# Kernel tuning notes

Hardware: AMD Instinct MI355X
Metric: run time of the kernel (lower is better)

## Reference

```python
import jax, jax.numpy as jnp
import numpy as np

B, C, H, W = 8, 512, 64, 64
C8 = C // 8


def setup_inputs() -> dict:
    key = jax.random.key(0)
    ks = jax.random.split(key, 9)
    s = 1.0 / np.sqrt(C)
    return {
        "view1": jax.random.normal(ks[0], (B, C, H, W), jnp.float32),
        "view2": jax.random.normal(ks[1], (B, C, H, W), jnp.float32),
        "Wq": jax.random.normal(ks[2], (C8, C), jnp.float32) * s,
        "bq": jax.random.normal(ks[3], (C8,), jnp.float32) * 0.01,
        "Wk": jax.random.normal(ks[4], (C8, C), jnp.float32) * s,
        "bk": jax.random.normal(ks[5], (C8,), jnp.float32) * 0.01,
        "Wv": jax.random.normal(ks[6], (C, C), jnp.float32) * s,
        "bv": jax.random.normal(ks[7], (C,), jnp.float32) * 0.01,
        "gamma": jnp.array([0.5], jnp.float32),  # nn.Parameter(zeros(1)) in torch; nonzero here for nontrivial output
    }


def reference(view1, view2, Wq, bq, Wk, bk, Wv, bv, gamma):
    b, c, h, w = view1.shape
    n = h * w
    # 1x1 convs == per-pixel linear over channel dim
    q = jnp.einsum("bchw,oc->bohw", view1, Wq) + bq[None, :, None, None]
    k = jnp.einsum("bchw,oc->bohw", view2, Wk) + bk[None, :, None, None]
    v = jnp.einsum("bchw,oc->bohw", view2, Wv) + bv[None, :, None, None]
    q = q.reshape(b, -1, n).transpose(0, 2, 1)  # (B, N, C/8)
    k = k.reshape(b, -1, n)                      # (B, C/8, N)
    v = v.reshape(b, c, n)                       # (B, C, N)
    # no scaling, matching the original module
    attn = jax.nn.softmax(jnp.einsum("bnd,bdm->bnm", q, k), axis=-1)  # (B, N, N)
    out = jnp.einsum("bcn,bmn->bcm", v, attn).reshape(b, c, h, w)
    return gamma[0] * out + view1
```

## Files before the change

### kernel.cpp

```cpp
#include <hip/hip_runtime.h>

#define NB 8
#define NC 512
#define NPIX 4096
#define LOG2E 1.44269504088896340736f
#define C0TERM 28.853900817779268f

typedef __attribute__((ext_vector_type(4))) float f32x4;
typedef __attribute__((ext_vector_type(8))) short bf16x8;
typedef __attribute__((ext_vector_type(4))) unsigned short u16x4;

static __device__ __forceinline__ short f2bf(float f){
    union { float f; unsigned u; } v; v.f = f;
    unsigned r = v.u + 0x7fffu + ((v.u >> 16) & 1u);
    return (short)(r >> 16);
}

static __device__ __forceinline__ void gload16(const void* g, void* l){
    __builtin_amdgcn_global_load_lds(
        (const __attribute__((address_space(1))) char*)g,
        (__attribute__((address_space(3))) char*)l, 16, 0, 0);
}

#define VW8 asm volatile("s_waitcnt vmcnt(8)" ::: "memory")
#define VW0 asm volatile("s_waitcnt vmcnt(0)" ::: "memory")
#define BAR __builtin_amdgcn_s_barrier()
#define SB0 __builtin_amdgcn_sched_barrier(0)

__global__ void k_wconv(const float* __restrict__ wq, const float* __restrict__ wk,
                        const float* __restrict__ wv,
                        short* __restrict__ wqb, short* __restrict__ wkb,
                        short* __restrict__ wvb){
    int i = blockIdx.x * 256 + threadIdx.x;
    if (i < 64*NC){ wqb[i] = f2bf(wq[i]); wkb[i] = f2bf(wk[i]); }
    if (i < NC*NC){ wvb[i] = f2bf(wv[i]); }
}

__global__ __launch_bounds__(256) void k_projq(const float* __restrict__ X,
                                               const short* __restrict__ W,
                                               const float* __restrict__ bias,
                                               short* __restrict__ out){
    const int b = blockIdx.y;
    const int wv = threadIdx.x >> 6;
    const int lane = threadIdx.x & 63;
    const int g = lane >> 4, c16 = lane & 15;
    const int n0w = blockIdx.x * 64 + wv * 16;
    const float* Xb = X + (size_t)b * NC * NPIX;

    f32x4 acc[4];
#pragma unroll
    for (int f = 0; f < 4; ++f) acc[f] = (f32x4){0.f,0.f,0.f,0.f};

    for (int c0 = 0; c0 < NC; c0 += 32){
        bf16x8 a;
#pragma unroll
        for (int j = 0; j < 8; ++j)
            a[j] = f2bf(Xb[(size_t)(c0 + 8*g + j) * NPIX + n0w + c16]);
#pragma unroll
        for (int f = 0; f < 4; ++f){
            bf16x8 bfr = *(const bf16x8*)(W + (size_t)(f*16 + c16) * NC + c0 + 8*g);
            acc[f] = __builtin_amdgcn_mfma_f32_16x16x32_bf16(a, bfr, acc[f], 0, 0, 0);
        }
    }
#pragma unroll
    for (int f = 0; f < 4; ++f){
        int o = f*16 + c16;
        float bo = bias[o];
#pragma unroll
        for (int i = 0; i < 4; ++i)
            out[((size_t)b*NPIX + n0w + 4*g + i)*64 + o] = f2bf(acc[f][i] + bo);
    }
}

__global__ __launch_bounds__(256) void k_trans(const float* __restrict__ X,
                                               short* __restrict__ Xt){
    __shared__ __align__(16) short T[64][72];
    const int n0 = blockIdx.x * 64;
    const int c0 = blockIdx.y * 64;
    const int b  = blockIdx.z;
    const int t  = threadIdx.x;
    {
        const int cl = t >> 2;
        const int nq = (t & 3) * 16;
        const float* src = X + ((size_t)b*NC + c0 + cl)*NPIX + n0 + nq;
#pragma unroll
        for (int q = 0; q < 4; ++q){
            f32x4 v = *(const f32x4*)(src + q*4);
#pragma unroll
            for (int i = 0; i < 4; ++i)
                T[nq + q*4 + i][cl] = f2bf(v[i]);
        }
    }
    __syncthreads();
    {
        const int n  = t >> 2;
        const int cs = (t & 3) * 16;
        short* dst = Xt + ((size_t)b*NPIX + n0 + n)*NC + c0 + cs;
        *(f32x4*)dst       = *(const f32x4*)&T[n][cs];
        *(f32x4*)(dst + 8) = *(const f32x4*)&T[n][cs + 8];
    }
}

__global__ __launch_bounds__(256) void k_projv(const short* __restrict__ Xt,
                                               const short* __restrict__ W,
                                               const float* __restrict__ bias,
                                               short* __restrict__ vout){
    const int o0 = blockIdx.x * 128;
    const int n0 = blockIdx.y * 128;
    const int b  = blockIdx.z;
    const int wv = threadIdx.x >> 6;
    const int lane = threadIdx.x & 63;
    const int g = lane >> 4, c16 = lane & 15;
    const int wo = wv & 1, wn = wv >> 1;

    const short* Xb = Xt + ((size_t)b*NPIX + n0 + wn*64)*NC;
    const short* Wb = W + (size_t)(o0 + wo*64)*NC;

    f32x4 acc[4][4];
#pragma unroll
    for (int nf = 0; nf < 4; ++nf)
#pragma unroll
        for (int of = 0; of < 4; ++of) acc[nf][of] = (f32x4){0.f,0.f,0.f,0.f};

    for (int c0 = 0; c0 < NC; c0 += 32){
        bf16x8 af[4], bf_[4];
#pragma unroll
        for (int f = 0; f < 4; ++f){
            af[f]  = *(const bf16x8*)(Xb + (size_t)(f*16 + c16)*NC + c0 + 8*g);
            bf_[f] = *(const bf16x8*)(Wb + (size_t)(f*16 + c16)*NC + c0 + 8*g);
        }
#pragma unroll
        for (int nf = 0; nf < 4; ++nf)
#pragma unroll
            for (int of = 0; of < 4; ++of)
                acc[nf][of] = __builtin_amdgcn_mfma_f32_16x16x32_bf16(af[nf], bf_[of], acc[nf][of], 0,0,0);
    }

#pragma unroll
    for (int of = 0; of < 4; ++of){
        int o = o0 + wo*64 + of*16 + c16;
        float bo = bias[o];
#pragma unroll
        for (int nf = 0; nf < 4; ++nf){
            int n = n0 + wn*64 + nf*16 + 4*g;
            u16x4 pk;
#pragma unroll
            for (int i = 0; i < 4; ++i) pk[i] = (unsigned short)f2bf(acc[nf][of][i] + bo);
            *(u16x4*)(vout + ((size_t)b*NC + o)*NPIX + n) = pk;
        }
    }
}

__global__ __launch_bounds__(256) void k_projk(const short* __restrict__ Xt,
                                               const short* __restrict__ W,
                                               const float* __restrict__ bias,
                                               short* __restrict__ kout){
    const int n0 = blockIdx.x * 256;
    const int b  = blockIdx.y;
    const int wv = threadIdx.x >> 6;
    const int lane = threadIdx.x & 63;
    const int g = lane >> 4, c16 = lane & 15;

    const short* Xb = Xt + ((size_t)b*NPIX + n0 + wv*64)*NC;

    f32x4 acc[4][4];
#pragma unroll
    for (int of = 0; of < 4; ++of)
#pragma unroll
        for (int nf = 0; nf < 4; ++nf) acc[of][nf] = (f32x4){0.f,0.f,0.f,0.f};

    for (int c0 = 0; c0 < NC; c0 += 32){
        bf16x8 af[4], bf_[4];
#pragma unroll
        for (int f = 0; f < 4; ++f){
            af[f]  = *(const bf16x8*)(W + (size_t)(f*16 + c16)*NC + c0 + 8*g);
            bf_[f] = *(const bf16x8*)(Xb + (size_t)(f*16 + c16)*NC + c0 + 8*g);
        }
#pragma unroll
        for (int of = 0; of < 4; ++of)
#pragma unroll
            for (int nf = 0; nf < 4; ++nf)
                acc[of][nf] = __builtin_amdgcn_mfma_f32_16x16x32_bf16(af[of], bf_[nf], acc[of][nf], 0,0,0);
    }

#pragma unroll
    for (int nf = 0; nf < 4; ++nf){
        int n = n0 + wv*64 + nf*16 + c16;
#pragma unroll
        for (int of = 0; of < 4; ++of){
            int o = of*16 + 4*g;
            u16x4 pk;
#pragma unroll
            for (int i = 0; i < 4; ++i) pk[i] = (unsigned short)f2bf(acc[of][nf][i] + bias[o+i]);
            *(u16x4*)(kout + ((size_t)b*NPIX + n)*64 + o) = pk;
        }
    }
}

__global__ __launch_bounds__(256) void k_projkv(const float* __restrict__ X,
                                                const short* __restrict__ Wv_,
                                                const float* __restrict__ bv_,
                                                const short* __restrict__ Wk_,
                                                const float* __restrict__ bk_,
                                                short* __restrict__ vout,
                                                short* __restrict__ kout){
    const int b = blockIdx.y;
    const int wv = threadIdx.x >> 6;
    const int lane = threadIdx.x & 63;
    const int g = lane >> 4, c16 = lane & 15;
    const int n0w = blockIdx.x * 32 + (wv & 1) * 16;
    const int oh = wv >> 1;
    const int o0v = oh * 256;
    const int o0k = oh * 32;
    const float* Xb = X + (size_t)b * NC * NPIX;

    f32x4 accv[16], acck[2];
#pragma unroll
    for (int f = 0; f < 16; ++f) accv[f] = (f32x4){0.f,0.f,0.f,0.f};
#pragma unroll
    for (int f = 0; f < 2;  ++f) acck[f] = (f32x4){0.f,0.f,0.f,0.f};

    for (int c0 = 0; c0 < NC; c0 += 32){
        bf16x8 a;
#pragma unroll
        for (int j = 0; j < 8; ++j)
            a[j] = f2bf(Xb[(size_t)(c0 + 8*g + j) * NPIX + n0w + c16]);
#pragma unroll
        for (int f = 0; f < 16; ++f){
            bf16x8 bfr = *(const bf16x8*)(Wv_ + (size_t)(o0v + f*16 + c16) * NC + c0 + 8*g);
            accv[f] = __builtin_amdgcn_mfma_f32_16x16x32_bf16(a, bfr, accv[f], 0, 0, 0);
        }
#pragma unroll
        for (int f = 0; f < 2; ++f){
            bf16x8 bfr = *(const bf16x8*)(Wk_ + (size_t)(o0k + f*16 + c16) * NC + c0 + 8*g);
            acck[f] = __builtin_amdgcn_mfma_f32_16x16x32_bf16(a, bfr, acck[f], 0, 0, 0);
        }
    }
#pragma unroll
    for (int f = 0; f < 16; ++f){
        int o = o0v + f*16 + c16;
        float bo = bv_[o];
        u16x4 pk;
#pragma unroll
        for (int i = 0; i < 4; ++i) pk[i] = (unsigned short)f2bf(accv[f][i] + bo);
        *(u16x4*)(vout + ((size_t)b*NC + o)*NPIX + n0w + 4*g) = pk;
    }
#pragma unroll
    for (int f = 0; f < 2; ++f){
        int o = o0k + f*16 + c16;
        float bo = bk_[o];
#pragma unroll
        for (int i = 0; i < 4; ++i)
            kout[((size_t)b*NPIX + n0w + 4*g + i)*64 + o] = f2bf(acck[f][i] + bo);
    }
}

__global__ __launch_bounds__(256) void k_qk(const short* __restrict__ qb,
                                            const short* __restrict__ kb,
                                            short* __restrict__ P,
                                            float* __restrict__ Lpart,
                                            int b0){
    __shared__ __align__(16) short Pt[64*256];
    const int m0 = blockIdx.x * 64;
    const int n0 = blockIdx.y * 256;
    const int bz = blockIdx.z;
    const int b  = b0 + bz;
    const int wv = threadIdx.x >> 6;
    const int lane = threadIdx.x & 63;
    const int g = lane >> 4, c16 = lane & 15;
    const int nsub = wv * 64;

    bf16x8 qf[4][2];
#pragma unroll
    for (int mf = 0; mf < 4; ++mf)
#pragma unroll
        for (int kk = 0; kk < 2; ++kk)
            qf[mf][kk] = *(const bf16x8*)(qb + ((size_t)b*NPIX + m0 + mf*16 + c16)*64 + kk*32 + 8*g);

    float lsum[4] = {0.f,0.f,0.f,0.f};
    char* Ptb = (char*)Pt;

#pragma unroll
    for (int nf = 0; nf < 4; ++nf){
        bf16x8 kf0 = *(const bf16x8*)(kb + ((size_t)b*NPIX + n0 + nsub + nf*16 + c16)*64 + 8*g);
        bf16x8 kf1 = *(const bf16x8*)(kb + ((size_t)b*NPIX + n0 + nsub + nf*16 + c16)*64 + 32 + 8*g);
#pragma unroll
        for (int mf = 0; mf < 4; ++mf){
            f32x4 s = (f32x4){0.f,0.f,0.f,0.f};
            s = __builtin_amdgcn_mfma_f32_16x16x32_bf16(kf0, qf[mf][0], s, 0,0,0);
            s = __builtin_amdgcn_mfma_f32_16x16x32_bf16(kf1, qf[mf][1], s, 0,0,0);
            u16x4 pk;
#pragma unroll
            for (int i = 0; i < 4; ++i){
                float p = exp2f(fmaf(s[i], LOG2E, -C0TERM));
                lsum[mf] += p;
                pk[i] = (unsigned short)f2bf(p);
            }
            int m = mf*16 + c16;
            int ncol = nsub + nf*16 + 4*g;
            *(u16x4*)(Ptb + m*512 + ((2*ncol) ^ ((m&7)<<4))) = pk;
        }
    }
    __syncthreads();

    {
        char* Pgb = (char*)(P + ((size_t)bz*NPIX + m0)*NPIX + n0);
        const int chunk = threadIdx.x & 31;
        const int row8  = threadIdx.x >> 5;
#pragma unroll
        for (int p = 0; p < 8; ++p){
            int row = p*8 + row8;
            f32x4 v = *(const f32x4*)(Ptb + row*512 + ((chunk*16) ^ ((row&7)<<4)));
            *(f32x4*)(Pgb + (size_t)row*(NPIX*2) + chunk*16) = v;
        }
    }

#pragma unroll
    for (int mf = 0; mf < 4; ++mf){
        lsum[mf] += __shfl_xor(lsum[mf], 16);
        lsum[mf] += __shfl_xor(lsum[mf], 32);
    }
    if (lane < 16){
        size_t base = ((size_t)bz*64 + blockIdx.y*4 + wv)*NPIX + m0 + lane;
#pragma unroll
        for (int mf = 0; mf < 4; ++mf)
            Lpart[base + mf*16] = lsum[mf];
    }
}

__global__ __launch_bounds__(256) void k_lred(const float* __restrict__ Lpart,
                                              const float* __restrict__ gamma,
                                              float* __restrict__ scale){
    int idx = blockIdx.x * 256 + threadIdx.x;
    int bz = idx >> 12, m = idx & 4095;
    float s = 0.f;
    for (int sl = 0; sl < 64; ++sl)
        s += Lpart[((size_t)bz*64 + sl)*NPIX + m];
    scale[idx] = gamma[0] / s;
}

__global__ __launch_bounds__(256) void k_pv(const short* __restrict__ vb,
                                            const short* __restrict__ P,
                                            const float* __restrict__ scale,
                                            const float* __restrict__ view1,
                                            float* __restrict__ out,
                                            int b0){
    __shared__ __align__(16) short At[2][128*64];
    __shared__ __align__(16) short Bt[2][128*64];
    const int p  = blockIdx.x + 4*blockIdx.y;
    const int mt = (p & 7) | (((p >> 5) & 3) << 3);
    const int ct = (p >> 3) & 3;
    const int c0 = ct * 128;
    const int m0 = mt * 128;
    const int bz = blockIdx.z;
    const int b  = b0 + bz;
    const int wv = threadIdx.x >> 6;
    const int lane = threadIdx.x & 63;
    const int g = lane >> 4, c16 = lane & 15;
    const int wc = wv & 1, wm = wv >> 1;
    const int lrow = lane >> 3;
    const int srcg = (lane & 7) ^ lrow;
    const int swz  = (c16 & 7) << 4;

    const char* Vg = (const char*)(vb + ((size_t)b*NC + c0)*NPIX);
    const char* Pg = (const char*)(P + ((size_t)bz*NPIX + m0)*NPIX);

    f32x4 acc[4][4];
#pragma unroll
    for (int cf = 0; cf < 4; ++cf)
#pragma unroll
        for (int mf = 0; mf < 4; ++mf) acc[cf][mf] = (f32x4){0.f,0.f,0.f,0.f};

    auto stage = [&](int buf, int t){
        size_t nbyte = (size_t)t * 64 * 2;
#pragma unroll
        for (int j = 0; j < 4; ++j){
            int r0 = wv*32 + j*8;
            int row = r0 + lrow;
            gload16(Vg + (size_t)row*(NPIX*2) + nbyte + srcg*16, (char*)&At[buf][0] + r0*128);
            gload16(Pg + (size_t)row*(NPIX*2) + nbyte + srcg*16, (char*)&Bt[buf][0] + r0*128);
        }
    };

    auto kstep = [&](int buf){
        const char* A  = (const char*)&At[buf][0];
        const char* Bp = (const char*)&Bt[buf][0];
#pragma unroll
        for (int kk = 0; kk < 2; ++kk){
            bf16x8 af[4], bfm[4];
#pragma unroll
            for (int f = 0; f < 4; ++f){
                af[f]  = *(const bf16x8*)(A  + (wc*64 + f*16 + c16)*128 + ((kk*64 + g*16) ^ swz));
                bfm[f] = *(const bf16x8*)(Bp + (wm*64 + f*16 + c16)*128 + ((kk*64 + g*16) ^ swz));
            }
            __builtin_amdgcn_s_setprio(1);
#pragma unroll
            for (int cf = 0; cf < 4; ++cf)
#pragma unroll
                for (int mf = 0; mf < 4; ++mf)
                    acc[cf][mf] = __builtin_amdgcn_mfma_f32_16x16x32_bf16(af[cf], bfm[mf], acc[cf][mf], 0,0,0);
            __builtin_amdgcn_s_setprio(0);
        }
    };

    stage(0, 0);
    stage(1, 1);

    for (int t2 = 0; t2 < 31; ++t2){
        VW8; BAR; SB0;
        kstep(0);
        BAR;
        stage(0, 2*t2 + 2);
        VW8; BAR; SB0;
        kstep(1);
        BAR;
        stage(1, 2*t2 + 3);
    }
    VW8; BAR; SB0;
    kstep(0);
    VW0; BAR; SB0;
    kstep(1);

    float sc[4];
#pragma unroll
    for (int mf = 0; mf < 4; ++mf)
        sc[mf] = scale[(size_t)bz*NPIX + m0 + wm*64 + mf*16 + c16];
#pragma unroll
    for (int cf = 0; cf < 4; ++cf){
#pragma unroll
        for (int mf = 0; mf < 4; ++mf){
            int m = m0 + wm*64 + mf*16 + c16;
#pragma unroll
            for (int i = 0; i < 4; ++i){
                int c = c0 + wc*64 + cf*16 + 4*g + i;
                size_t idx = ((size_t)b*NC + c)*NPIX + m;
                out[idx] = sc[mf]*acc[cf][mf][i] + view1[idx];
            }
        }
    }
}

__global__ __launch_bounds__(512, 2) void k_attn(const short* __restrict__ qb,
                                                 const short* __restrict__ kb,
                                                 const short* __restrict__ vb,
                                                 const float* __restrict__ view1,
                                                 const float* __restrict__ gamma,
                                                 float* __restrict__ out){
    __shared__ __align__(16) short P[2][64*64];
    __shared__ float Lred[128];

    const int bid = blockIdx.x;
    const int b  = bid & 7;
    const int m0 = (bid >> 3) * 64;
    const int wv = threadIdx.x >> 6;
    const int lane = threadIdx.x & 63;
    const int g = lane >> 4, c16 = lane & 15;
    const int msubA = (wv & 3) * 16;
    const int nhalf = wv >> 2;
    const int c0w = wv * 64;

    const short* qrow = qb + ((size_t)b*NPIX + m0 + msubA + c16)*64 + 8*g;
    bf16x8 qa0 = *(const bf16x8*)qrow;
    bf16x8 qa1 = *(const bf16x8*)(qrow + 32);

    const size_t kbase = (size_t)b * NPIX * 64;
    const int mrow = msubA + c16;
    const int swz = (mrow & 7) << 4;
    float Lacc = 0.f;

    f32x4 acc[4][4];
#pragma unroll
    for (int f = 0; f < 4; ++f)
#pragma unroll
        for (int cf = 0; cf < 4; ++cf) acc[f][cf] = (f32x4){0.f,0.f,0.f,0.f};

    char* Pb0 = (char*)&P[0][0];
    char* Pb1 = (char*)&P[1][0];

    bf16x8 vrA[8], vrB[8], krA[4], krB[4];

    auto loadK = [&](int t, bf16x8 (&kr)[4]){
        const short* kp = kb + kbase + (size_t)(t*64 + nhalf*32 + c16)*64 + 8*g;
        kr[0] = *(const bf16x8*)kp;
        kr[1] = *(const bf16x8*)(kp + 32);
        kr[2] = *(const bf16x8*)(kp + 16*64);
        kr[3] = *(const bf16x8*)(kp + 16*64 + 32);
    };
    auto loadV = [&](int t, bf16x8 (&vr)[8]){
#pragma unroll
        for (int h = 0; h < 2; ++h)
#pragma unroll
            for (int cf = 0; cf < 4; ++cf)
                vr[h*4+cf] = *(const bf16x8*)(vb + ((size_t)b*NC + c0w + cf*16 + c16)*NPIX
                                              + t*64 + h*32 + 8*g);
    };

    auto compA = [&](bf16x8 kA, bf16x8 kB, int fn, char* pb){
        f32x4 s = (f32x4){0.f,0.f,0.f,0.f};
        s = __builtin_amdgcn_mfma_f32_16x16x32_bf16(kA, qa0, s, 0,0,0);
        s = __builtin_amdgcn_mfma_f32_16x16x32_bf16(kB, qa1, s, 0,0,0);
        u16x4 pk;
#pragma unroll
        for (int i = 0; i < 4; ++i){
            float p = exp2f(fmaf(s[i], LOG2E, -C0TERM));
            Lacc += p;
            pk[i] = (unsigned short)f2bf(p);
        }
        int nrel0 = nhalf*32 + fn*16 + 4*g;
        *(u16x4*)(pb + mrow*128 + ((2*nrel0) ^ swz)) = pk;
    };

    auto phaseB = [&](const char* pc, const bf16x8 (&vr)[8]){
#pragma unroll
        for (int h = 0; h < 2; ++h){
            bf16x8 pa[4];
#pragma unroll
            for (int f = 0; f < 4; ++f){
                int row = f*16 + c16;
                pa[f] = *(const bf16x8*)(pc + row*128 + ((h*64 + g*16) ^ ((row&7)<<4)));
            }
#pragma unroll
            for (int cf = 0; cf < 4; ++cf)
#pragma unroll
                for (int f = 0; f < 4; ++f)
                    acc[f][cf] = __builtin_amdgcn_mfma_f32_16x16x32_bf16(pa[f], vr[h*4+cf], acc[f][cf], 0,0,0);
        }
    };

    auto iter = [&](int t, char* bufA, const char* bufB,
                    const bf16x8 (&vcur)[8], bf16x8 (&vnext)[8],
                    const bf16x8 (&kcur)[4], bf16x8 (&knext)[4]){
        loadV(t+1, vnext);
        loadK(t+2 < 64 ? t+2 : 63, knext);
        __builtin_amdgcn_s_setprio(1);
        phaseB(bufB, vcur);
        __builtin_amdgcn_s_setprio(0);
        compA(kcur[0], kcur[1], 0, bufA);
        compA(kcur[2], kcur[3], 1, bufA);
        asm volatile("s_waitcnt lgkmcnt(0)" ::: "memory");
        __builtin_amdgcn_s_barrier();
    };

    loadV(0, vrA);
    loadK(0, krA);
    loadK(1, krB);
    compA(krA[0], krA[1], 0, Pb0);
    compA(krA[2], krA[3], 1, Pb0);
    asm volatile("s_waitcnt lgkmcnt(0)" ::: "memory");
    __builtin_amdgcn_s_barrier();

    for (int t2 = 0; t2 < 31; ++t2){
        iter(2*t2,     Pb1, Pb0, vrA, vrB, krB, krA);
        iter(2*t2 + 1, Pb0, Pb1, vrB, vrA, krA, krB);
    }
    iter(62, Pb1, Pb0, vrA, vrB, krB, krA);
    __builtin_amdgcn_s_setprio(1);
    phaseB(Pb1, vrB);
    __builtin_amdgcn_s_setprio(0);

    Lacc += __shfl_xor(Lacc, 16);
    Lacc += __shfl_xor(Lacc, 32);
    if (lane < 16) Lred[nhalf*64 + msubA + lane] = Lacc;
    __syncthreads();

    float gm = gamma[0];
#pragma unroll
    for (int f = 0; f < 4; ++f){
        float sc[4];
#pragma unroll
        for (int i = 0; i < 4; ++i){
            int r = f*16 + 4*g + i;
            float Ls = Lred[r] + Lred[64 + r];
            sc[i] = gm / Ls;
        }
#pragma unroll
        for (int cf = 0; cf < 4; ++cf){
            int c = c0w + cf*16 + c16;
            size_t base = ((size_t)b*NC + c)*NPIX + m0 + f*16 + 4*g;
            f32x4 v1 = *(const f32x4*)(view1 + base);
            f32x4 r;
#pragma unroll
            for (int i = 0; i < 4; ++i) r[i] = sc[i]*acc[f][cf][i] + v1[i];
            *(f32x4*)(out + base) = r;
        }
    }
}

extern "C" void kernel_launch(void* const* d_in, const int* in_sizes, int n_in,
                              void* d_out, int out_size, void* d_ws, size_t ws_size,
                              hipStream_t stream){
    const float* view1 = (const float*)d_in[0];
    const float* view2 = (const float*)d_in[1];
    const float* Wq    = (const float*)d_in[2];
    const float* bq    = (const float*)d_in[3];
    const float* Wk    = (const float*)d_in[4];
    const float* bk    = (const float*)d_in[5];
    const float* Wv    = (const float*)d_in[6];
    const float* bv    = (const float*)d_in[7];
    const float* gamma = (const float*)d_in[8];
    float* out = (float*)d_out;

    char* ws = (char*)d_ws;
    short* qbuf = (short*)(ws);
    short* kbuf = (short*)(ws + (size_t)4*1024*1024);
    short* vbuf = (short*)(ws + (size_t)8*1024*1024);
    short* wqb  = (short*)(ws + (size_t)40*1024*1024);
    short* wkb  = (short*)(ws + (size_t)40*1024*1024 + 64*1024);
    short* wvb  = (short*)(ws + (size_t)40*1024*1024 + 128*1024);
    float* scl  = (float*)(ws + (size_t)41*1024*1024);
    float* Lpart= (float*)(ws + (size_t)42*1024*1024);
    short* Pbuf = (short*)(ws + (size_t)50*1024*1024);
    short* X2t  = Pbuf;
    short* X1t  = Pbuf + (size_t)16*1024*1024;

    const size_t FIXED = (size_t)50*1024*1024;
    const size_t PPB   = (size_t)NPIX*NPIX*2;
    int avail = 0;
    if (ws_size > FIXED){
        size_t nn = (ws_size - FIXED) / PPB;
        avail = nn > 8 ? 8 : (int)nn;
    }
    int nbc = (avail >= 8) ? 8 : (avail >= 4) ? 4 : (avail >= 2) ? 2 : avail;

    hipLaunchKernelGGL(k_wconv, dim3(1024), dim3(256), 0, stream, Wq, Wk, Wv, wqb, wkb, wvb);

    if (nbc >= 1){
        hipLaunchKernelGGL(k_trans, dim3(64, 8, 8), dim3(256), 0, stream, view2, X2t);
        hipLaunchKernelGGL(k_projv, dim3(4, 32, 8), dim3(256), 0, stream, X2t, wvb, bv, vbuf);
        hipLaunchKernelGGL(k_projk, dim3(16, 8),    dim3(256), 0, stream, X2t, wkb, bk, kbuf);
        if (nbc >= 2){
            hipLaunchKernelGGL(k_trans, dim3(64, 8, 8), dim3(256), 0, stream, view1, X1t);
            hipLaunchKernelGGL(k_projk, dim3(16, 8),    dim3(256), 0, stream, X1t, wqb, bq, qbuf);
        } else {
            hipLaunchKernelGGL(k_projq, dim3(64, 8), dim3(256), 0, stream, view1, wqb, bq, qbuf);
        }
        for (int b0 = 0; b0 < NB; b0 += nbc){
            int nb = (NB - b0 < nbc) ? (NB - b0) : nbc;
            hipLaunchKernelGGL(k_qk,   dim3(64, 16, nb), dim3(256), 0, stream, qbuf, kbuf, Pbuf, Lpart, b0);
            hipLaunchKernelGGL(k_lred, dim3(nb*16),      dim3(256), 0, stream, Lpart, gamma, scl);
            hipLaunchKernelGGL(k_pv,   dim3(4, 32, nb),  dim3(256), 0, stream, vbuf, Pbuf, scl, view1, out, b0);
        }
    } else {
        hipLaunchKernelGGL(k_projq,  dim3(64, 8),  dim3(256), 0, stream, view1, wqb, bq, qbuf);
        hipLaunchKernelGGL(k_projkv, dim3(128, 8), dim3(256), 0, stream, view2, wvb, bv, wkb, bk, vbuf, kbuf);
        hipLaunchKernelGGL(k_attn, dim3(512), dim3(512), 0, stream, qbuf, kbuf, vbuf, view1, gamma, out);
    }
}
```

Measured before the change: 421.6 us.

## Load V operand directly into registers in PV GEMM, bypassing LDS

The PV kernel no longer stages V tiles through shared memory. Each lane now loads its V MFMA fragments straight from global memory into registers, one k-step ahead, while P tiles still go through double-buffered LDS via direct global-to-LDS loads. The goal is to halve LDS capacity and LDS read traffic and to drop the separate V LDS reads. In exchange, global V reads are less coalesced, fewer loads are in flight ahead of use, and the scheduling barriers that used to control instruction order are gone.

After: 552.7 us. 31.1% more time.

```diff
diff --git a/kernel.cpp b/kernel.cpp
--- a/kernel.cpp
+++ b/kernel.cpp
@@ -21,11 +21,6 @@
         (const __attribute__((address_space(1))) char*)g,
         (__attribute__((address_space(3))) char*)l, 16, 0, 0);
 }
-
-#define VW8 asm volatile("s_waitcnt vmcnt(8)" ::: "memory")
-#define VW0 asm volatile("s_waitcnt vmcnt(0)" ::: "memory")
-#define BAR __builtin_amdgcn_s_barrier()
-#define SB0 __builtin_amdgcn_sched_barrier(0)
 
 __global__ void k_wconv(const float* __restrict__ wq, const float* __restrict__ wk,
                         const float* __restrict__ wv,
@@ -345,7 +340,6 @@
                                             const float* __restrict__ view1,
                                             float* __restrict__ out,
                                             int b0){
-    __shared__ __align__(16) short At[2][128*64];
     __shared__ __align__(16) short Bt[2][128*64];
     const int p  = blockIdx.x + 4*blockIdx.y;
     const int mt = (p & 7) | (((p >> 5) & 3) << 3);
@@ -362,8 +356,11 @@
     const int srcg = (lane & 7) ^ lrow;
     const int swz  = (c16 & 7) << 4;
 
-    const char* Vg = (const char*)(vb + ((size_t)b*NC + c0)*NPIX);
     const char* Pg = (const char*)(P + ((size_t)bz*NPIX + m0)*NPIX);
+    const short* Vp[4];
+#pragma unroll
+    for (int f = 0; f < 4; ++f)
+        Vp[f] = vb + ((size_t)b*NC + c0 + wc*64 + f*16 + c16)*NPIX + 8*g;
 
     f32x4 acc[4][4];
 #pragma unroll
@@ -371,54 +368,63 @@
 #pragma unroll
         for (int mf = 0; mf < 4; ++mf) acc[cf][mf] = (f32x4){0.f,0.f,0.f,0.f};
 
+    bf16x8 vr[8];
+
     auto stage = [&](int buf, int t){
-        size_t nbyte = (size_t)t * 64 * 2;
+        size_t nbyte = (size_t)t * 128;
 #pragma unroll
         for (int j = 0; j < 4; ++j){
             int r0 = wv*32 + j*8;
             int row = r0 + lrow;
-            gload16(Vg + (size_t)row*(NPIX*2) + nbyte + srcg*16, (char*)&At[buf][0] + r0*128);
             gload16(Pg + (size_t)row*(NPIX*2) + nbyte + srcg*16, (char*)&Bt[buf][0] + r0*128);
         }
     };
-
+    auto loadV = [&](int t){
+#pragma unroll
+        for (int kk = 0; kk < 2; ++kk)
+#pragma unroll
+            for (int cf = 0; cf < 4; ++cf)
+                vr[kk*4+cf] = *(const bf16x8*)(Vp[cf] + (size_t)t*64 + kk*32);
+    };
     auto kstep = [&](int buf){
-        const char* A  = (const char*)&At[buf][0];
         const char* Bp = (const char*)&Bt[buf][0];
 #pragma unroll
         for (int kk = 0; kk < 2; ++kk){
-            bf16x8 af[4], bfm[4];
-#pragma unroll
-            for (int f = 0; f < 4; ++f){
-                af[f]  = *(const bf16x8*)(A  + (wc*64 + f*16 + c16)*128 + ((kk*64 + g*16) ^ swz));
+            bf16x8 bfm[4];
+#pragma unroll
+            for (int f = 0; f < 4; ++f)
                 bfm[f] = *(const bf16x8*)(Bp + (wm*64 + f*16 + c16)*128 + ((kk*64 + g*16) ^ swz));
-            }
             __builtin_amdgcn_s_setprio(1);
 #pragma unroll
             for (int cf = 0; cf < 4; ++cf)
 #pragma unroll
                 for (int mf = 0; mf < 4; ++mf)
-                    acc[cf][mf] = __builtin_amdgcn_mfma_f32_16x16x32_bf16(af[cf], bfm[mf], acc[cf][mf], 0,0,0);
+                    acc[cf][mf] = __builtin_amdgcn_mfma_f32_16x16x32_bf16(vr[kk*4+cf], bfm[mf], acc[cf][mf], 0,0,0);
             __builtin_amdgcn_s_setprio(0);
         }
     };
 
     stage(0, 0);
-    stage(1, 1);
+    loadV(0);
+    __syncthreads();
 
     for (int t2 = 0; t2 < 31; ++t2){
-        VW8; BAR; SB0;
+        stage(1, 2*t2 + 1);
         kstep(0);
-        BAR;
+        loadV(2*t2 + 1);
+        asm volatile("s_waitcnt vmcnt(8) lgkmcnt(0)" ::: "memory");
+        __builtin_amdgcn_s_barrier();
         stage(0, 2*t2 + 2);
-        VW8; BAR; SB0;
         kstep(1);
-        BAR;
-        stage(1, 2*t2 + 3);
-    }
-    VW8; BAR; SB0;
+        loadV(2*t2 + 2);
+        asm volatile("s_waitcnt vmcnt(8) lgkmcnt(0)" ::: "memory");
+        __builtin_amdgcn_s_barrier();
+    }
+    stage(1, 63);
     kstep(0);
-    VW0; BAR; SB0;
+    loadV(63);
+    asm volatile("s_waitcnt vmcnt(8) lgkmcnt(0)" ::: "memory");
+    __builtin_amdgcn_s_barrier();
     kstep(1);
 
     float sc[4];
```
